# Performance work log

Hardware: AMD Instinct MI355X
Metric: run time of the kernel (lower is better)

## Reference

```python
import jax, jax.numpy as jnp
import numpy as np

B, S, TK, H, E, V, OOV = 16, 8, 400, 256, 128, 50000, 50
H2 = 2 * H


def setup_inputs() -> dict:
    key = jax.random.key(0)
    ks = jax.random.split(key, 24)
    std = 0.02
    d = {}
    d["y_t_1"] = jax.random.randint(ks[0], (B,), 0, V)
    d["h0"] = jax.random.normal(ks[1], (B, H), jnp.float32)
    d["c0"] = jax.random.normal(ks[2], (B, H), jnp.float32)
    d["encoder_output"] = jax.random.normal(ks[3], (B, S, TK, H2), jnp.float32)
    d["section_output"] = jax.random.normal(ks[4], (B, S, H2), jnp.float32)
    d["enc_padding_mask"] = jnp.ones((B, S, TK), jnp.float32)
    d["c_t_1"] = jax.random.normal(ks[5], (B, H2), jnp.float32)
    d["extra_zeros"] = jnp.zeros((B, OOV), jnp.float32)
    d["enc_batch_extend_vocab"] = jax.random.randint(ks[6], (B, S * TK), 0, V + OOV)
    d["coverage"] = jnp.zeros((B, S, TK), jnp.float32)
    d["gamma"] = jnp.ones((B, S, TK), jnp.float32)
    # learned parameters
    d["embedding"] = std * jax.random.normal(ks[7], (V, E), jnp.float32)
    d["W_xc"] = std * jax.random.normal(ks[8], (H2 + E, E), jnp.float32)
    d["b_xc"] = jnp.zeros((E,), jnp.float32)
    d["W_ih"] = std * jax.random.normal(ks[9], (E, 4 * H), jnp.float32)
    d["b_ih"] = jnp.zeros((4 * H,), jnp.float32)
    d["W_hh"] = std * jax.random.normal(ks[10], (H, 4 * H), jnp.float32)
    # pytorch init sets forget-gate bias (2nd quarter) to 1
    d["b_hh"] = jnp.zeros((4 * H,), jnp.float32).at[H:2 * H].set(1.0)
    d["Wh_sec"] = std * jax.random.normal(ks[11], (H2, H2), jnp.float32)
    d["Wd_sec"] = std * jax.random.normal(ks[12], (H2, H2), jnp.float32)
    d["bd_sec"] = jnp.zeros((H2,), jnp.float32)
    d["v_sec"] = std * jax.random.normal(ks[13], (H2, 1), jnp.float32)
    d["Wh_w"] = std * jax.random.normal(ks[14], (H2, H2), jnp.float32)
    d["Wc_w"] = std * jax.random.normal(ks[15], (H2,), jnp.float32)
    d["Wd_w"] = std * jax.random.normal(ks[16], (H2, H2), jnp.float32)
    d["bd_w"] = jnp.zeros((H2,), jnp.float32)
    d["v_w"] = std * jax.random.normal(ks[17], (H2, 1), jnp.float32)
    d["W_pgen"] = std * jax.random.normal(ks[18], (4 * H + E, 1), jnp.float32)
    d["b_pgen"] = jnp.zeros((1,), jnp.float32)
    d["W_out1"] = std * jax.random.normal(ks[19], (3 * H, H), jnp.float32)
    d["b_out1"] = jnp.zeros((H,), jnp.float32)
    d["W_out2"] = std * jax.random.normal(ks[20], (H, V), jnp.float32)
    d["b_out2"] = jnp.zeros((V,), jnp.float32)
    return d


def reference(y_t_1, h0, c0, encoder_output, section_output, enc_padding_mask,
              c_t_1, extra_zeros, enc_batch_extend_vocab, coverage, gamma,
              embedding, W_xc, b_xc, W_ih, b_ih, W_hh, b_hh,
              Wh_sec, Wd_sec, bd_sec, v_sec,
              Wh_w, Wc_w, Wd_w, bd_w, v_w,
              W_pgen, b_pgen, W_out1, b_out1, W_out2, b_out2):
    # embedding + input context projection
    emb = embedding[y_t_1]                                      # [B,E]
    x = jnp.concatenate([c_t_1, emb], axis=1) @ W_xc + b_xc     # [B,E]
    # single-step LSTM (pytorch gate order i,f,g,o)
    gates = x @ W_ih + b_ih + h0 @ W_hh + b_hh                  # [B,4H]
    i, f, g, o = jnp.split(gates, 4, axis=1)
    c = jax.nn.sigmoid(f) * c0 + jax.nn.sigmoid(i) * jnp.tanh(g)
    h = jax.nn.sigmoid(o) * jnp.tanh(c)
    s_t_hat = jnp.concatenate([h, c], axis=1)                   # [B,2H]
    # section attention -> beta [B,S]
    e_sec = jnp.tanh(section_output @ Wh_sec + (s_t_hat @ Wd_sec + bd_sec)[:, None, :])
    sc_sec = jnp.squeeze(e_sec @ v_sec, -1)                     # [B,S]
    beta = jax.nn.softmax(sc_sec, axis=1)
    beta = beta / beta.sum(axis=1, keepdims=True)
    # word attention with coverage feature
    att = encoder_output @ Wh_w + (s_t_hat @ Wd_w + bd_w)[:, None, None, :]
    att = att + coverage[..., None] * Wc_w                      # [B,S,TK,2H]
    sc_w = jnp.squeeze(jnp.tanh(att) @ v_w, -1)                 # [B,S,TK]
    ws = (beta[:, :, None] * sc_w).reshape(B, S * TK)
    mask = enc_padding_mask.reshape(B, S * TK)
    ad = jax.nn.softmax(ws, axis=1) * mask
    attn = ad / ad.sum(axis=1, keepdims=True)                   # [B,S*TK]
    c_t = jnp.einsum('bt,btn->bn', attn, encoder_output.reshape(B, S * TK, H2))
    cov = coverage + attn.reshape(B, S, TK)
    # pointer-gen gate
    p_gen = jax.nn.sigmoid(jnp.concatenate([c_t, s_t_hat, x], axis=1) @ W_pgen + b_pgen)  # [B,1]
    # output vocab distribution
    out = jnp.concatenate([h, c_t], axis=1) @ W_out1 + b_out1
    vocab_dist = jax.nn.softmax(out @ W_out2 + b_out2, axis=1)  # [B,V]
    vd = jnp.concatenate([p_gen * vocab_dist, extra_zeros], axis=1)  # [B,V+OOV]
    ad_ = (1.0 - p_gen) * attn
    rows = jnp.arange(B)[:, None]
    final_dist = vd.at[rows, enc_batch_extend_vocab].add(ad_)
    return (final_dist, h, c, c_t, attn, p_gen, cov)
```

## Files before the change

kernel.cpp:

```cpp
#include <hip/hip_runtime.h>
#include <math.h>

#define BB   16
#define SS   8
#define TKK  400
#define HH   256
#define EE   128
#define VV   50000
#define OOVV 50
#define HH2  512
#define STK  (SS*TKK)
#define VOO  (VV+OOVV)

#define OFF_X     0
#define OFF_ST    2048
#define OFF_SD    10240
#define OFF_WD    18432
#define OFF_SCSEC 26752
#define OFF_SCW   26880
#define OFF_CT    78080
#define OFF_OUT1  86272
#define OFF_PGEN  90368
#define OFF_PSUM  93520
#define OFF_BT    113040

#define O_FD   0
#define O_H    800800
#define O_C    804896
#define O_CT   808992
#define O_ATTN 817184
#define O_PGEN 868384
#define O_COV  868400

#define NLB 391
#define GEMM_NB 800

typedef __attribute__((ext_vector_type(8))) short bf16x8;
typedef __attribute__((ext_vector_type(4))) float f32x4;

__device__ __forceinline__ float sigm(float x){ return 1.0f/(1.0f+expf(-x)); }

__device__ __forceinline__ unsigned short f2b(float f){
  unsigned int u = __float_as_uint(f);
  unsigned int r = (u + 0x7fffu + ((u >> 16) & 1u)) >> 16;
  return (unsigned short)r;
}

__device__ __forceinline__ float tanhfast(float x){
  float cx = fminf(9.0f, fmaxf(-9.0f, x));
  float t = __expf(2.0f*cx);
  return (t - 1.0f) * __builtin_amdgcn_rcpf(t + 1.0f);
}

__device__ __forceinline__ float wave_sum(float v){
  #pragma unroll
  for(int o=32;o>0;o>>=1) v += __shfl_xor(v,o);
  return v;
}
__device__ __forceinline__ float wave_max(float v){
  #pragma unroll
  for(int o=32;o>0;o>>=1) v = fmaxf(v,__shfl_xor(v,o));
  return v;
}

__device__ __forceinline__ void glds16(const void* g, void* l){
  __builtin_amdgcn_global_load_lds((const __attribute__((address_space(1))) void*)g,
                                   (__attribute__((address_space(3))) void*)l, 16, 0, 0);
}

__device__ __forceinline__ bf16x8 cvt8(float4 a, float4 b){
  union{ bf16x8 v; unsigned short u[8]; } t;
  t.u[0]=f2b(a.x); t.u[1]=f2b(a.y); t.u[2]=f2b(a.z); t.u[3]=f2b(a.w);
  t.u[4]=f2b(b.x); t.u[5]=f2b(b.y); t.u[6]=f2b(b.z); t.u[7]=f2b(b.w);
  return t.v;
}

__global__ void k_pre(const float* __restrict__ Whw, unsigned short* __restrict__ Btg,
                      const int* __restrict__ y, const float* __restrict__ ct1,
                      const float* __restrict__ emb, const float* __restrict__ Wxc,
                      const float* __restrict__ bxc, float* __restrict__ ws){
  __shared__ float sm[10440];
  int bi = blockIdx.x, tid = threadIdx.x;
  if(bi < 64){
    int n0 = (bi & 7)*64, k0 = (bi >> 3)*64;
    int tx = tid & 63, ty = tid >> 6;
    #pragma unroll
    for(int it=0; it<16; it++){
      int kk = it*4 + ty;
      sm[kk*65 + tx] = Whw[(size_t)(k0+kk)*HH2 + n0 + tx];
    }
    __syncthreads();
    #pragma unroll
    for(int it=0; it<2; it++){
      int kgl = it*4 + ty;
      int kgG = (k0 >> 3) + kgl;
      int rnd = kgG >> 2, kg = kgG & 3;
      int col = n0 + tx;
      union{ bf16x8 v; unsigned short u[8]; } t;
      #pragma unroll
      for(int j=0;j<8;j++) t.u[j] = f2b(sm[(kgl*8+j)*65 + tx]);
      *(bf16x8*)&Btg[(size_t)rnd*16384 + (size_t)(col*4 + (kg ^ ((col>>1)&3)))*8] = t.v;
    }
  } else if(bi < 80){
    float* cat = sm;
    float* red = sm + 10240;
    for(int f=tid; f<BB*640; f+=256){
      int b = f/640, r = f - b*640;
      cat[f] = (r < HH2) ? ct1[b*HH2 + r] : emb[(size_t)y[b]*EE + (r-HH2)];
    }
    __syncthreads();
    int c = (bi-64)*8 + (tid & 7);
    int b = (tid >> 3) & 15;
    int kh = tid >> 7;
    float acc = 0.0f;
    const float* a = &cat[b*640];
    for(int k=kh*320; k<kh*320+320; k++) acc += a[k]*Wxc[k*EE + c];
    if(kh==1) red[b*8 + (tid&7)] = acc;
    __syncthreads();
    if(kh==0) ws[OFF_X + b*EE + c] = acc + red[b*8 + (tid&7)] + bxc[c];
  } else {
    for(int f=tid; f<BB*HH2; f+=256) ws[OFF_CT + f] = 0.0f;
  }
}

__global__ void k_lstm(const float* __restrict__ h0, const float* __restrict__ c0,
                       const float* __restrict__ Wih, const float* __restrict__ bih,
                       const float* __restrict__ Whh, const float* __restrict__ bhh,
                       float* __restrict__ ws, float* __restrict__ out){
  __shared__ float xh[4*384];
  __shared__ float red[3*64*4];
  int tid = threadIdx.x;
  int jc = (blockIdx.x & 15)*16, bc = (blockIdx.x >> 4)*4;
  for(int f=tid; f<4*384; f+=256){
    int bl = f/384, r = f - bl*384;
    xh[f] = (r < EE) ? ws[OFF_X + (bc+bl)*EE + r] : h0[(bc+bl)*HH + (r-EE)];
  }
  __syncthreads();
  int jl = tid & 15, bl = (tid >> 4) & 3, kq = tid >> 6;
  int j = jc + jl, b = bc + bl;
  float a0=0.f, a1=0.f, a2=0.f, a3=0.f;
  const float* a = &xh[bl*384];
  for(int k=kq*96; k<kq*96+96; k++){
    float v = a[k];
    const float* w = (k < EE) ? &Wih[k*4*HH + j] : &Whh[(k-EE)*4*HH + j];
    a0 += v*w[0]; a1 += v*w[HH]; a2 += v*w[2*HH]; a3 += v*w[3*HH];
  }
  if(kq){
    float* r = &red[((kq-1)*64 + bl*16 + jl)*4];
    r[0]=a0; r[1]=a1; r[2]=a2; r[3]=a3;
  }
  __syncthreads();
  if(kq==0){
    #pragma unroll
    for(int p=0;p<3;p++){
      const float* r = &red[(p*64 + bl*16 + jl)*4];
      a0+=r[0]; a1+=r[1]; a2+=r[2]; a3+=r[3];
    }
    a0 += bih[j] + bhh[j];
    a1 += bih[j+HH] + bhh[j+HH];
    a2 += bih[j+2*HH] + bhh[j+2*HH];
    a3 += bih[j+3*HH] + bhh[j+3*HH];
    float c = sigm(a1)*c0[b*HH+j] + sigm(a0)*tanhf(a2);
    float h = sigm(a3)*tanhf(c);
    out[O_H + b*HH + j] = h;
    out[O_C + b*HH + j] = c;
    ws[OFF_ST + b*HH2 + j]      = h;
    ws[OFF_ST + b*HH2 + HH + j] = c;
  }
}

__global__ void k_proj(const float* __restrict__ Wdsec, const float* __restrict__ bdsec,
                       const float* __restrict__ Wdw,  const float* __restrict__ bdw,
                       float* __restrict__ ws){
  __shared__ float st[BB*HH2];
  __shared__ float red[128];
  int tid = threadIdx.x;
  for(int f=tid; f<BB*HH2; f+=256) st[f] = ws[OFF_ST + f];
  __syncthreads();
  int mi = blockIdx.x >> 6;
  int c = (blockIdx.x & 63)*8 + (tid & 7);
  int bl = (tid >> 3) & 15;
  int kq = tid >> 7;
  const float* Wm = mi ? Wdw : Wdsec;
  const float* bias = mi ? bdw : bdsec;
  int dst = mi ? OFF_WD : OFF_SD;
  float acc = 0.0f;
  const float* a = &st[bl*HH2];
  for(int k=kq*256; k<kq*256+256; k++) acc += a[k]*Wm[k*HH2 + c];
  if(kq==1) red[bl*8 + (tid&7)] = acc;
  __syncthreads();
  if(kq==0) ws[dst + bl*HH2 + c] = acc + red[bl*8 + (tid&7)] + bias[c];
}

__global__ __launch_bounds__(512, 4) void k_gemm6(
        const float* __restrict__ A, const unsigned short* __restrict__ Btg,
        const float* __restrict__ Wcw, const float* __restrict__ vw,
        const float* __restrict__ cover,
        const float* __restrict__ sec, const float* __restrict__ Whsec,
        const float* __restrict__ vsec, float* __restrict__ ws){
  __shared__ __align__(16) unsigned short smem[32768];
  int tid = threadIdx.x;
  if(blockIdx.x >= GEMM_NB){
    float* row = (float*)smem;
    float* red = row + HH2;
    int bi = blockIdx.x - GEMM_NB;
    int b = bi >> 3;
    if(tid < HH2) row[tid] = sec[(size_t)bi*HH2 + tid];
    __syncthreads();
    int col = tid;
    float acc = 0.0f;
    #pragma unroll 8
    for(int k=0;k<HH2;k++) acc += row[k]*Whsec[k*HH2 + col];
    float val = tanhf(acc + ws[OFF_SD + b*HH2 + col]) * vsec[col];
    val = wave_sum(val);
    if((tid&63)==0) red[tid>>6] = val;
    __syncthreads();
    if(tid==0){
      float s = 0.0f;
      #pragma unroll
      for(int i=0;i<8;i++) s += red[i];
      ws[OFF_SCSEC + bi] = s;
    }
    return;
  }
  int w = tid >> 6, lane = tid & 63, m = lane & 15, q = lane >> 4;
  int mk = (m >> 1) & 3, sw = q ^ mk;
  int rg = w >> 1, cg = w & 1;
  int row0 = blockIdx.x * 64;
  int b = blockIdx.x / 50;

  const float* arow_p = &A[(size_t)(row0 + rg*16 + m)*HH2 + q*8];

  f32x4 acc[16];
  #pragma unroll
  for(int j=0;j<16;j++) acc[j] = (f32x4){0.f,0.f,0.f,0.f};

  #define GLDSB(rr, bufsel) {                                                  \
    const unsigned short* bsrc_ = Btg + (size_t)(rr)*16384;                    \
    _Pragma("unroll")                                                          \
    for(int i_=0;i_<4;i_++)                                                    \
      glds16(bsrc_ + i_*4096 + tid*8, &smem[(bufsel)*16384 + i_*4096 + tid*8]);\
  }

  GLDSB(0, 0);
  float4 pa0 = *(const float4*)(arow_p);
  float4 pa1 = *(const float4*)(arow_p + 4);
  GLDSB(1, 1);
  asm volatile("s_waitcnt vmcnt(6)" ::: "memory");
  __builtin_amdgcn_sched_barrier(0);
  bf16x8 af = cvt8(pa0, pa1);
  __builtin_amdgcn_s_barrier();

  #pragma unroll
  for(int r=0; r<16; r++){
    if(r < 15){
      pa0 = *(const float4*)(arow_p + (r+1)*32);
      pa1 = *(const float4*)(arow_p + (r+1)*32 + 4);
    }
    __builtin_amdgcn_s_setprio(1);
    #pragma unroll
    for(int cf=0; cf<16; cf++){
      int col = cg*256 + cf*16 + m;
      bf16x8 bv = *(const bf16x8*)&smem[(size_t)(r&1)*16384 + ((size_t)col*4 + sw)*8];
      acc[cf] = __builtin_amdgcn_mfma_f32_16x16x32_bf16(af, bv, acc[cf], 0,0,0);
    }
    __builtin_amdgcn_s_setprio(0);
    if(r < 14){
      asm volatile("s_waitcnt lgkmcnt(0)" ::: "memory");
      __builtin_amdgcn_sched_barrier(0);
      __builtin_amdgcn_s_barrier();
      GLDSB(r+2, (r&1));
    }
    if(r < 15){
      if(r < 14){ asm volatile("s_waitcnt vmcnt(6)" ::: "memory"); }
      else      { asm volatile("s_waitcnt vmcnt(2)" ::: "memory"); }
      __builtin_amdgcn_sched_barrier(0);
      af = cvt8(pa0, pa1);
      __builtin_amdgcn_s_barrier();
    }
  }
  #undef GLDSB

  float cov[4];
  #pragma unroll
  for(int r=0;r<4;r++) cov[r] = cover[row0 + rg*16 + q*4 + r];
  float rsum[4] = {0,0,0,0};
  #pragma unroll
  for(int j=0;j<16;j++){
    int col = cg*256 + j*16 + m;
    float wdv = ws[OFF_WD + b*HH2 + col];
    float wcv = Wcw[col], vwv = vw[col];
    #pragma unroll
    for(int r=0;r<4;r++)
      rsum[r] += tanhfast(acc[j][r] + wdv + cov[r]*wcv) * vwv;
  }
  __syncthreads();
  float* rbuf = (float*)smem;
  #pragma unroll
  for(int r=0;r<4;r++){
    float v = rsum[r];
    v += __shfl_xor(v,1,16); v += __shfl_xor(v,2,16);
    v += __shfl_xor(v,4,16); v += __shfl_xor(v,8,16);
    if(m==0) rbuf[cg*64 + rg*16 + q*4 + r] = v;
  }
  __syncthreads();
  if(tid < 64) ws[OFF_SCW + row0 + tid] = rbuf[tid] + rbuf[64 + tid];
}

__global__ void k_attn(const float* __restrict__ mask, const float* __restrict__ cover,
                       float* __restrict__ ws, float* __restrict__ out){
  int b = blockIdx.x, tid = threadIdx.x;
  __shared__ float vals[STK];
  __shared__ float red[4];
  __shared__ float sc[SS];
  if(tid < SS) sc[tid] = ws[OFF_SCSEC + b*SS + tid];
  __syncthreads();
  float bm = -1e30f;
  #pragma unroll
  for(int s=0;s<SS;s++) bm = fmaxf(bm, sc[s]);
  float be[SS]; float bsum = 0.0f;
  #pragma unroll
  for(int s=0;s<SS;s++){ be[s] = expf(sc[s]-bm); bsum += be[s]; }
  #pragma unroll
  for(int s=0;s<SS;s++) be[s] /= bsum;
  int lane = tid & 63, w = tid >> 6;
  float m = -1e30f;
  for(int j=tid;j<STK;j+=256){
    float v = be[j/TKK] * ws[OFF_SCW + b*STK + j];
    vals[j] = v; m = fmaxf(m, v);
  }
  m = wave_max(m);
  if(lane==0) red[w] = m;
  __syncthreads();
  m = fmaxf(fmaxf(red[0],red[1]), fmaxf(red[2],red[3]));
  __syncthreads();
  float ssum = 0.0f;
  for(int j=tid;j<STK;j+=256){
    float e = expf(vals[j]-m) * mask[b*STK + j];
    vals[j] = e; ssum += e;
  }
  ssum = wave_sum(ssum);
  if(lane==0) red[w] = ssum;
  __syncthreads();
  float inv = 1.0f/(red[0]+red[1]+red[2]+red[3]);
  for(int j=tid;j<STK;j+=256){
    float a = vals[j]*inv;
    out[O_ATTN + b*STK + j] = a;
    out[O_COV  + b*STK + j] = cover[b*STK + j] + a;
  }
}

__global__ void k_ct(const float* __restrict__ enc, const float* __restrict__ out,
                     float* __restrict__ ws){
  int b = blockIdx.y, tid = threadIdx.x;
  __shared__ float a[64];
  __shared__ float part[512];
  int t0 = blockIdx.x*64;
  if(tid<64) a[tid] = out[O_ATTN + b*STK + t0 + tid];
  __syncthreads();
  int c4 = tid & 127, rh = tid >> 7;
  const float4* e4 = (const float4*)enc;
  size_t base = ((size_t)(b*STK + t0 + rh*32))*128 + c4;
  float4 acc = {0.f,0.f,0.f,0.f};
  #pragma unroll 8
  for(int rr=0; rr<32; rr++){
    float4 v = e4[base + (size_t)rr*128];
    float av = a[rh*32 + rr];
    acc.x += av*v.x; acc.y += av*v.y; acc.z += av*v.z; acc.w += av*v.w;
  }
  if(rh) *(float4*)&part[c4*4] = acc;
  __syncthreads();
  if(!rh){
    float4 o = *(const float4*)&part[c4*4];
    atomicAdd(&ws[OFF_CT + b*HH2 + c4*4 + 0], acc.x + o.x);
    atomicAdd(&ws[OFF_CT + b*HH2 + c4*4 + 1], acc.y + o.y);
    atomicAdd(&ws[OFF_CT + b*HH2 + c4*4 + 2], acc.z + o.z);
    atomicAdd(&ws[OFF_CT + b*HH2 + c4*4 + 3], acc.w + o.w);
  }
}

__global__ void k_out1(const float* __restrict__ Wp, const float* __restrict__ bp,
                       const float* __restrict__ Wo1, const float* __restrict__ bo1,
                       float* __restrict__ ws, float* __restrict__ out){
  __shared__ float cat[BB*768];
  __shared__ float red[3*64];
  int tid = threadIdx.x;
  if(blockIdx.x == 64){
    int w = tid >> 6, lane = tid & 63;
    #pragma unroll
    for(int i=0;i<4;i++){
      int b = w*4 + i;
      float p = 0.0f;
      for(int k=lane;k<4*HH+EE;k+=64){
        float val = (k < HH2) ? ws[OFF_CT + b*HH2 + k]
                  : (k < 4*HH) ? ws[OFF_ST + b*HH2 + (k-HH2)]
                  : ws[OFF_X + b*EE + (k-4*HH)];
        p += val * Wp[k];
      }
      p = wave_sum(p);
      if(lane==0){
        float pg = sigm(p + bp[0]);
        ws[OFF_PGEN + b] = pg;
        out[O_PGEN + b]  = pg;
      }
    }
    for(int f=tid; f<BB*HH2; f+=256) out[O_CT + f] = ws[OFF_CT + f];
    return;
  }
  for(int f=tid; f<BB*768; f+=256){
    int b = f/768, r = f - b*768;
    cat[f] = (r < HH) ? ws[OFF_ST + b*HH2 + r] : ws[OFF_CT + b*HH2 + (r-HH)];
  }
  __syncthreads();
  int cl = tid & 3, bl = (tid >> 2) & 15, kq = tid >> 6;
  int c = blockIdx.x*4 + cl;
  float acc = 0.0f;
  const float* a = &cat[bl*768];
  for(int k=kq*192; k<kq*192+192; k++) acc += a[k]*Wo1[k*HH + c];
  if(kq) red[(kq-1)*64 + bl*4 + cl] = acc;
  __syncthreads();
  if(kq==0){
    acc += red[bl*4+cl] + red[64 + bl*4+cl] + red[128 + bl*4+cl];
    ws[OFF_OUT1 + bl*HH + c] = acc + bo1[c];
  }
}

__global__ void k_logits(const float* __restrict__ W2, const float* __restrict__ b2,
                         float* __restrict__ ws, float* __restrict__ out){
  int tid = threadIdx.x;
  __shared__ float o1[BB*HH];
  for(int i=tid;i<BB*HH/4;i+=256)
    ((float4*)o1)[i] = ((const float4*)&ws[OFF_OUT1])[i];
  __syncthreads();
  int cl = tid & 31, bq = tid >> 5;
  int c4 = blockIdx.x*128 + cl*4;
  bool ok = c4 < VV;
  int b0 = bq*2, b1 = b0+1;
  float4 acc0 = {0.f,0.f,0.f,0.f}, acc1 = {0.f,0.f,0.f,0.f};
  if(ok){
    const float* oa = &o1[b0*HH];
    const float* ob = &o1[b1*HH];
    #pragma unroll 4
    for(int k=0;k<HH;k++){
      float4 wv = *(const float4*)&W2[(size_t)k*VV + c4];
      float xa = oa[k], xb = ob[k];
      acc0.x += xa*wv.x; acc0.y += xa*wv.y; acc0.z += xa*wv.z; acc0.w += xa*wv.w;
      acc1.x += xb*wv.x; acc1.y += xb*wv.y; acc1.z += xb*wv.z; acc1.w += xb*wv.w;
    }
  }
  float bv[4] = {0,0,0,0};
  if(ok){ float4 t = *(const float4*)&b2[c4]; bv[0]=t.x; bv[1]=t.y; bv[2]=t.z; bv[3]=t.w; }
  float a0[4] = {acc0.x, acc0.y, acc0.z, acc0.w};
  float a1[4] = {acc1.x, acc1.y, acc1.z, acc1.w};
  float s0 = 0.0f, s1 = 0.0f;
  #pragma unroll
  for(int j=0;j<4;j++){
    float e0 = ok ? expf(a0[j]+bv[j]) : 0.0f;
    float e1 = ok ? expf(a1[j]+bv[j]) : 0.0f;
    if(ok){
      out[(size_t)b0*VOO + c4 + j] = e0;
      out[(size_t)b1*VOO + c4 + j] = e1;
    }
    s0 += e0; s1 += e1;
  }
  #pragma unroll
  for(int o=1;o<32;o<<=1){ s0 += __shfl_xor(s0,o,32); s1 += __shfl_xor(s1,o,32); }
  if(cl==0){
    ws[OFF_PSUM + b0*NLB + blockIdx.x] = s0;
    ws[OFF_PSUM + b1*NLB + blockIdx.x] = s1;
  }
}

__global__ void k_final(const float* __restrict__ xz, float* __restrict__ ws,
                        float* __restrict__ out){
  int b = blockIdx.y;
  int v = blockIdx.x*256 + threadIdx.x;
  __shared__ float red[4];
  int lane = threadIdx.x & 63, w = threadIdx.x >> 6;
  float p = 0.0f;
  for(int i=threadIdx.x;i<NLB;i+=256) p += ws[OFF_PSUM + b*NLB + i];
  p = wave_sum(p);
  if(lane==0) red[w] = p;
  __syncthreads();
  float s = red[0]+red[1]+red[2]+red[3];
  float pg = ws[OFF_PGEN + b];
  if(v < VV)       out[(size_t)b*VOO + v] = pg * out[(size_t)b*VOO + v] / s;
  else if(v < VOO) out[(size_t)b*VOO + v] = xz[b*OOVV + (v-VV)];
}

__global__ void k_scatter(const int* __restrict__ ebev, float* __restrict__ ws,
                          float* __restrict__ out){
  int b = blockIdx.x;
  float r = 1.0f - ws[OFF_PGEN + b];
  for(int j=threadIdx.x;j<STK;j+=256){
    int idx = ebev[b*STK + j];
    atomicAdd(&out[(size_t)b*VOO + idx], r*out[O_ATTN + b*STK + j]);
  }
}

extern "C" void kernel_launch(void* const* d_in, const int* in_sizes, int n_in,
                              void* d_out, int out_size, void* d_ws, size_t ws_size,
                              hipStream_t stream){
  const int*   y     = (const int*)  d_in[0];
  const float* h0    = (const float*)d_in[1];
  const float* c0    = (const float*)d_in[2];
  const float* enc   = (const float*)d_in[3];
  const float* sec   = (const float*)d_in[4];
  const float* mask  = (const float*)d_in[5];
  const float* ct1   = (const float*)d_in[6];
  const float* xz    = (const float*)d_in[7];
  const int*   ebev  = (const int*)  d_in[8];
  const float* cover = (const float*)d_in[9];
  const float* emb   = (const float*)d_in[11];
  const float* Wxc   = (const float*)d_in[12];
  const float* bxc   = (const float*)d_in[13];
  const float* Wih   = (const float*)d_in[14];
  const float* bih   = (const float*)d_in[15];
  const float* Whh   = (const float*)d_in[16];
  const float* bhh   = (const float*)d_in[17];
  const float* Whsec = (const float*)d_in[18];
  const float* Wdsec = (const float*)d_in[19];
  const float* bdsec = (const float*)d_in[20];
  const float* vsec  = (const float*)d_in[21];
  const float* Whw   = (const float*)d_in[22];
  const float* Wcw   = (const float*)d_in[23];
  const float* Wdw   = (const float*)d_in[24];
  const float* bdw   = (const float*)d_in[25];
  const float* vw    = (const float*)d_in[26];
  const float* Wp    = (const float*)d_in[27];
  const float* bp    = (const float*)d_in[28];
  const float* Wo1   = (const float*)d_in[29];
  const float* bo1   = (const float*)d_in[30];
  const float* Wo2   = (const float*)d_in[31];
  const float* bo2   = (const float*)d_in[32];
  float* out = (float*)d_out;
  float* ws  = (float*)d_ws;
  unsigned short* Btg = (unsigned short*)(ws + OFF_BT);

  k_pre    <<<dim3(81),       dim3(256), 0, stream>>>(Whw, Btg, y, ct1, emb, Wxc, bxc, ws);
  k_lstm   <<<dim3(64),       dim3(256), 0, stream>>>(h0, c0, Wih, bih, Whh, bhh, ws, out);
  k_proj   <<<dim3(128),      dim3(256), 0, stream>>>(Wdsec, bdsec, Wdw, bdw, ws);
  k_gemm6  <<<dim3(928),      dim3(512), 0, stream>>>(enc, Btg, Wcw, vw, cover, sec, Whsec, vsec, ws);
  k_attn   <<<dim3(BB),       dim3(256), 0, stream>>>(mask, cover, ws, out);
  k_ct     <<<dim3(50,BB),    dim3(256), 0, stream>>>(enc, out, ws);
  k_out1   <<<dim3(65),       dim3(256), 0, stream>>>(Wp, bp, Wo1, bo1, ws, out);
  k_logits <<<dim3(NLB),      dim3(256), 0, stream>>>(Wo2, bo2, ws, out);
  k_final  <<<dim3(196,BB),   dim3(256), 0, stream>>>(xz, ws, out);
  k_scatter<<<dim3(BB),       dim3(256), 0, stream>>>(ebev, ws, out);
}
```

Baseline: 487.6 us.

## Split-K projection with atomics, parallelize attention softmax and scatter across blocks

The decoder-state projection is rewritten as a split-K kernel: each block handles 32 K rows for all 16 batches and accumulates into bias-preinitialized outputs with atomics. The single-block-per-batch attention softmax is split in two. One kernel spread over many blocks computes exp without max subtraction and accumulates the row sums atomically. Normalization, the attn output and the coverage update are folded into the context kernel. The scatter runs over more blocks per batch. This trades serialized low-occupancy kernels for more parallelism, at the cost of extra atomics and relying on attention scores being bounded for exp without max-shift to stay safe.

```diff
diff --git a/kernel.cpp b/kernel.cpp
--- a/kernel.cpp
+++ b/kernel.cpp
@@ -22,6 +22,7 @@
 #define OFF_OUT1  86272
 #define OFF_PGEN  90368
 #define OFF_PSUM  93520
+#define OFF_ASUM  99776
 #define OFF_BT    113040
 
 #define O_FD   0
@@ -57,11 +58,6 @@
   for(int o=32;o>0;o>>=1) v += __shfl_xor(v,o);
   return v;
 }
-__device__ __forceinline__ float wave_max(float v){
-  #pragma unroll
-  for(int o=32;o>0;o>>=1) v = fmaxf(v,__shfl_xor(v,o));
-  return v;
-}
 
 __device__ __forceinline__ void glds16(const void* g, void* l){
   __builtin_amdgcn_global_load_lds((const __attribute__((address_space(1))) void*)g,
@@ -78,7 +74,8 @@
 __global__ void k_pre(const float* __restrict__ Whw, unsigned short* __restrict__ Btg,
                       const int* __restrict__ y, const float* __restrict__ ct1,
                       const float* __restrict__ emb, const float* __restrict__ Wxc,
-                      const float* __restrict__ bxc, float* __restrict__ ws){
+                      const float* __restrict__ bxc, const float* __restrict__ bdsec,
+                      const float* __restrict__ bdw, float* __restrict__ ws){
   __shared__ float sm[10440];
   int bi = blockIdx.x, tid = threadIdx.x;
   if(bi < 64){
@@ -119,7 +116,13 @@
     __syncthreads();
     if(kh==0) ws[OFF_X + b*EE + c] = acc + red[b*8 + (tid&7)] + bxc[c];
   } else {
-    for(int f=tid; f<BB*HH2; f+=256) ws[OFF_CT + f] = 0.0f;
+    for(int f=tid; f<BB*HH2; f+=256){
+      int c = f & (HH2-1);
+      ws[OFF_CT + f] = 0.0f;
+      ws[OFF_SD + f] = bdsec[c];
+      ws[OFF_WD + f] = bdw[c];
+    }
+    if(tid < BB) ws[OFF_ASUM + tid] = 0.0f;
   }
 }
 
@@ -169,27 +172,33 @@
   }
 }
 
-__global__ void k_proj(const float* __restrict__ Wdsec, const float* __restrict__ bdsec,
-                       const float* __restrict__ Wdw,  const float* __restrict__ bdw,
+__global__ void k_proj(const float* __restrict__ Wdsec, const float* __restrict__ Wdw,
                        float* __restrict__ ws){
-  __shared__ float st[BB*HH2];
-  __shared__ float red[128];
+  __shared__ float st[BB*32];
   int tid = threadIdx.x;
-  for(int f=tid; f<BB*HH2; f+=256) st[f] = ws[OFF_ST + f];
-  __syncthreads();
-  int mi = blockIdx.x >> 6;
-  int c = (blockIdx.x & 63)*8 + (tid & 7);
-  int bl = (tid >> 3) & 15;
-  int kq = tid >> 7;
-  const float* Wm = mi ? Wdw : Wdsec;
-  const float* bias = mi ? bdw : bdsec;
+  int mi = blockIdx.x >> 5;
+  int cb = (blockIdx.x >> 4) & 1;
+  int kq = blockIdx.x & 15;
+  int k0 = kq*32;
+  for(int f=tid; f<BB*32; f+=256){
+    int b = f >> 5, kk = f & 31;
+    st[f] = ws[OFF_ST + b*HH2 + k0 + kk];
+  }
+  __syncthreads();
+  int c = cb*256 + tid;
+  const float* Wm = (mi ? Wdw : Wdsec) + (size_t)k0*HH2 + c;
+  float acc[BB];
+  #pragma unroll
+  for(int b=0;b<BB;b++) acc[b] = 0.0f;
+  #pragma unroll 4
+  for(int kk=0;kk<32;kk++){
+    float wv = Wm[(size_t)kk*HH2];
+    #pragma unroll
+    for(int b=0;b<BB;b++) acc[b] += st[b*32 + kk]*wv;
+  }
   int dst = mi ? OFF_WD : OFF_SD;
-  float acc = 0.0f;
-  const float* a = &st[bl*HH2];
-  for(int k=kq*256; k<kq*256+256; k++) acc += a[k]*Wm[k*HH2 + c];
-  if(kq==1) red[bl*8 + (tid&7)] = acc;
-  __syncthreads();
-  if(kq==0) ws[dst + bl*HH2 + c] = acc + red[bl*8 + (tid&7)] + bias[c];
+  #pragma unroll
+  for(int b=0;b<BB;b++) atomicAdd(&ws[dst + b*HH2 + c], acc[b]);
 }
 
 __global__ __launch_bounds__(512, 4) void k_gemm6(
@@ -307,56 +316,42 @@
   if(tid < 64) ws[OFF_SCW + row0 + tid] = rbuf[tid] + rbuf[64 + tid];
 }
 
-__global__ void k_attn(const float* __restrict__ mask, const float* __restrict__ cover,
-                       float* __restrict__ ws, float* __restrict__ out){
-  int b = blockIdx.x, tid = threadIdx.x;
-  __shared__ float vals[STK];
-  __shared__ float red[4];
-  __shared__ float sc[SS];
-  if(tid < SS) sc[tid] = ws[OFF_SCSEC + b*SS + tid];
-  __syncthreads();
+__global__ void k_attnA(const float* __restrict__ mask, float* __restrict__ ws,
+                        float* __restrict__ out){
+  int b = blockIdx.y;
+  int j = blockIdx.x*256 + threadIdx.x;
+  float sc[SS];
+  #pragma unroll
+  for(int s=0;s<SS;s++) sc[s] = ws[OFF_SCSEC + b*SS + s];
   float bm = -1e30f;
   #pragma unroll
   for(int s=0;s<SS;s++) bm = fmaxf(bm, sc[s]);
-  float be[SS]; float bsum = 0.0f;
-  #pragma unroll
-  for(int s=0;s<SS;s++){ be[s] = expf(sc[s]-bm); bsum += be[s]; }
-  #pragma unroll
-  for(int s=0;s<SS;s++) be[s] /= bsum;
-  int lane = tid & 63, w = tid >> 6;
-  float m = -1e30f;
-  for(int j=tid;j<STK;j+=256){
-    float v = be[j/TKK] * ws[OFF_SCW + b*STK + j];
-    vals[j] = v; m = fmaxf(m, v);
-  }
-  m = wave_max(m);
-  if(lane==0) red[w] = m;
-  __syncthreads();
-  m = fmaxf(fmaxf(red[0],red[1]), fmaxf(red[2],red[3]));
-  __syncthreads();
-  float ssum = 0.0f;
-  for(int j=tid;j<STK;j+=256){
-    float e = expf(vals[j]-m) * mask[b*STK + j];
-    vals[j] = e; ssum += e;
-  }
-  ssum = wave_sum(ssum);
-  if(lane==0) red[w] = ssum;
-  __syncthreads();
-  float inv = 1.0f/(red[0]+red[1]+red[2]+red[3]);
-  for(int j=tid;j<STK;j+=256){
-    float a = vals[j]*inv;
-    out[O_ATTN + b*STK + j] = a;
-    out[O_COV  + b*STK + j] = cover[b*STK + j] + a;
-  }
-}
-
-__global__ void k_ct(const float* __restrict__ enc, const float* __restrict__ out,
-                     float* __restrict__ ws){
+  float bsum = 0.0f;
+  #pragma unroll
+  for(int s=0;s<SS;s++){ sc[s] = expf(sc[s]-bm); bsum += sc[s]; }
+  float e = 0.0f;
+  if(j < STK){
+    float be = sc[j/TKK] / bsum;
+    e = expf(be * ws[OFF_SCW + b*STK + j]) * mask[b*STK + j];
+    out[O_ATTN + b*STK + j] = e;
+  }
+  float sv = wave_sum(e);
+  if((threadIdx.x & 63) == 0) atomicAdd(&ws[OFF_ASUM + b], sv);
+}
+
+__global__ void k_attnB(const float* __restrict__ enc, const float* __restrict__ cover,
+                        float* __restrict__ ws, float* __restrict__ out){
   int b = blockIdx.y, tid = threadIdx.x;
   __shared__ float a[64];
   __shared__ float part[512];
   int t0 = blockIdx.x*64;
-  if(tid<64) a[tid] = out[O_ATTN + b*STK + t0 + tid];
+  float inv = 1.0f / ws[OFF_ASUM + b];
+  if(tid < 64){
+    float av = out[O_ATTN + b*STK + t0 + tid] * inv;
+    a[tid] = av;
+    out[O_ATTN + b*STK + t0 + tid] = av;
+    out[O_COV  + b*STK + t0 + tid] = cover[b*STK + t0 + tid] + av;
+  }
   __syncthreads();
   int c4 = tid & 127, rh = tid >> 7;
   const float4* e4 = (const float4*)enc;
@@ -490,9 +485,9 @@
 
 __global__ void k_scatter(const int* __restrict__ ebev, float* __restrict__ ws,
                           float* __restrict__ out){
-  int b = blockIdx.x;
+  int b = blockIdx.y;
   float r = 1.0f - ws[OFF_PGEN + b];
-  for(int j=threadIdx.x;j<STK;j+=256){
+  for(int j=blockIdx.x*256+threadIdx.x;j<STK;j+=1024){
     int idx = ebev[b*STK + j];
     atomicAdd(&out[(size_t)b*VOO + idx], r*out[O_ATTN + b*STK + j]);
   }
@@ -537,14 +532,14 @@
   float* ws  = (float*)d_ws;
   unsigned short* Btg = (unsigned short*)(ws + OFF_BT);
 
-  k_pre    <<<dim3(81),       dim3(256), 0, stream>>>(Whw, Btg, y, ct1, emb, Wxc, bxc, ws);
-  k_lstm   <<<dim3(64),       dim3(256), 0, stream>>>(h0, c0, Wih, bih, Whh, bhh, ws, out);
-  k_proj   <<<dim3(128),      dim3(256), 0, stream>>>(Wdsec, bdsec, Wdw, bdw, ws);
-  k_gemm6  <<<dim3(928),      dim3(512), 0, stream>>>(enc, Btg, Wcw, vw, cover, sec, Whsec, vsec, ws);
-  k_attn   <<<dim3(BB),       dim3(256), 0, stream>>>(mask, cover, ws, out);
-  k_ct     <<<dim3(50,BB),    dim3(256), 0, stream>>>(enc, out, ws);
-  k_out1   <<<dim3(65),       dim3(256), 0, stream>>>(Wp, bp, Wo1, bo1, ws, out);
-  k_logits <<<dim3(NLB),      dim3(256), 0, stream>>>(Wo2, bo2, ws, out);
-  k_final  <<<dim3(196,BB),   dim3(256), 0, stream>>>(xz, ws, out);
-  k_scatter<<<dim3(BB),       dim3(256), 0, stream>>>(ebev, ws, out);
-}
+  k_pre    <<<dim3(81),       dim3(256),  0, stream>>>(Whw, Btg, y, ct1, emb, Wxc, bxc, bdsec, bdw, ws);
+  k_lstm   <<<dim3(64),       dim3(256),  0, stream>>>(h0, c0, Wih, bih, Whh, bhh, ws, out);
+  k_proj   <<<dim3(64),       dim3(256),  0, stream>>>(Wdsec, Wdw, ws);
+  k_gemm6  <<<dim3(928),      dim3(512),  0, stream>>>(enc, Btg, Wcw, vw, cover, sec, Whsec, vsec, ws);
+  k_attnA  <<<dim3(13,BB),    dim3(256),  0, stream>>>(mask, ws, out);
+  k_attnB  <<<dim3(50,BB),    dim3(256),  0, stream>>>(enc, cover, ws, out);
+  k_out1   <<<dim3(65),       dim3(256),  0, stream>>>(Wp, bp, Wo1, bo1, ws, out);
+  k_logits <<<dim3(NLB),      dim3(256),  0, stream>>>(Wo2, bo2, ws, out);
+  k_final  <<<dim3(196,BB),   dim3(256),  0, stream>>>(xz, ws, out);
+  k_scatter<<<dim3(4,BB),     dim3(256),  0, stream>>>(ebev, ws, out);
+}
```

After: 466.2 us. -4.4%, faster.
